# Performance work log

Measured on AMD Instinct MI355X. Metric: run time of the kernel, lower is better.

The kernel has to match this reference:

```python
import jax, jax.numpy as jnp
import numpy as np

INF = 1e+24
DK = 16


def setup_inputs() -> dict:
    key = jax.random.key(0)
    ks = jax.random.split(key, 9)
    B, T, D = 64, 512, 1024
    x = jax.random.normal(ks[0], (B, T, D), dtype=jnp.float32)
    padding_mask = jax.random.randint(ks[1], (B, T, 1), 0, 2) > 0
    s = 1.0 / np.sqrt(D)
    Wq = jax.random.normal(ks[2], (D, DK), dtype=jnp.float32) * s
    bq = jnp.zeros((DK,), dtype=jnp.float32)
    Wk = jax.random.normal(ks[3], (D, DK), dtype=jnp.float32) * s
    bk = jnp.zeros((DK,), dtype=jnp.float32)
    Wv = jax.random.normal(ks[4], (D, D), dtype=jnp.float32) * s
    bv = jnp.zeros((D,), dtype=jnp.float32)
    return {"x": x, "padding_mask": padding_mask, "Wq": Wq, "bq": bq,
            "Wk": Wk, "bk": bk, "Wv": Wv, "bv": bv}


def reference(x, padding_mask, Wq, bq, Wk, bk, Wv, bv):
    # x: [B,T,D]; padding_mask: [B,T,1] bool
    q = x @ Wq + bq                      # [B,T,dk]
    k = x @ Wk + bk                      # [B,T,dk]
    v = x @ Wv + bv                      # [B,T,D]
    # original writes -INF into k at padded positions (broadcast over dk)
    k = jnp.where(padding_mask, jnp.float32(-INF), k)
    # NOTE: original multiplies by sqrt(dk) (misnamed _inv_dk)
    att = jnp.einsum('btd,bsd->bts', q, k) * jnp.sqrt(jnp.float32(DK))
    T = x.shape[1]
    causal = jnp.triu(jnp.ones((T, T), dtype=bool), k=1)  # [T,T]
    att = jnp.where(causal[None, :, :], jnp.float32(-INF), att)
    return jnp.einsum('bts,bsd->btd', jax.nn.softmax(att, axis=2), v)
```

## Files before the change

kernel.cpp:

```cpp
#include <hip/hip_runtime.h>
#include <hip/hip_bf16.h>
#include <stdint.h>

#define NEG_BIG (-1e24f)

typedef __attribute__((ext_vector_type(8))) short bf16x8;
typedef __attribute__((ext_vector_type(4))) float f32x4;

#define AS1 __attribute__((address_space(1)))
#define AS3 __attribute__((address_space(3)))

__device__ __forceinline__ void gload_lds16(const void* g, void* l) {
    __builtin_amdgcn_global_load_lds((AS1 unsigned*)g, (AS3 unsigned*)l, 16, 0, 0);
}

__device__ __forceinline__ unsigned short f2bf(float f) {
    union { float f; unsigned u; } v; v.f = f;
    return (unsigned short)((v.u + 0x7FFFu + ((v.u >> 16) & 1u)) >> 16);
}

__global__ void detect_mask_kernel(const unsigned* pm, int* flag) {
    __shared__ int notI, notF;
    if (threadIdx.x == 0) { notI = 0; notF = 0; }
    __syncthreads();
    int li = 0, lf = 0;
    for (int i = threadIdx.x; i < 8192; i += 256) {
        unsigned v = pm[i];
        if (v > 1u) li = 1;
        if (v != 0u && v != 0x3F800000u) lf = 1;
    }
    if (li) atomicOr(&notI, 1);
    if (lf) atomicOr(&notF, 1);
    __syncthreads();
    if (threadIdx.x == 0) *flag = notI ? (notF ? 1 : 2) : 0;
}

__global__ __launch_bounds__(1024, 8)
void qk_conv_kernel(const float* __restrict__ x,
                    const float* __restrict__ Wq, const float* __restrict__ bq,
                    const float* __restrict__ Wk, const float* __restrict__ bk,
                    const void* __restrict__ pm, const int* __restrict__ pmflag,
                    unsigned short* __restrict__ xbf,
                    float* __restrict__ qo, float* __restrict__ ko) {
    __shared__ float smem[4 * 64 * 33];
    float* xs = smem;
    const int tid = threadIdx.x;
    const int r0 = blockIdx.x * 64;
    const int lane = tid & 63;
    const int wv = __builtin_amdgcn_readfirstlane(tid >> 6);
    const int g = wv & 3;
    const int sl = wv >> 2;
    const int jb = (g & 1) * 8;
    const int d0 = sl * 16;
    const float* __restrict__ W = (g < 2) ? Wq : Wk;

    const int sr = tid >> 4;
    const int sd = (tid & 15) * 4;
    const float* __restrict__ xp = x + (size_t)(r0 + sr) * 1024 + sd;
    unsigned short* __restrict__ xbp = xbf + (size_t)(r0 + sr) * 1024 + sd;

    float acc[8];
#pragma unroll
    for (int j = 0; j < 8; j++) acc[j] = 0.f;

    float4 xv = *(const float4*)xp;
    for (int c0 = 0; c0 < 1024; c0 += 64) {
        uint2 pk;
        pk.x = (unsigned)f2bf(xv.x) | ((unsigned)f2bf(xv.y) << 16);
        pk.y = (unsigned)f2bf(xv.z) | ((unsigned)f2bf(xv.w) << 16);
        *(uint2*)(xbp + c0) = pk;
        xs[sr * 65 + sd + 0] = xv.x;
        xs[sr * 65 + sd + 1] = xv.y;
        xs[sr * 65 + sd + 2] = xv.z;
        xs[sr * 65 + sd + 3] = xv.w;
        __syncthreads();
        if (c0 + 64 < 1024) xv = *(const float4*)(xp + c0 + 64);
        const float* __restrict__ wrow = W + (size_t)(c0 + d0) * 16 + jb;
        const float* __restrict__ xrow = xs + lane * 65 + d0;
#pragma unroll 4
        for (int dd = 0; dd < 16; dd++) {
            const float xvv = xrow[dd];
            const float* __restrict__ w = wrow + (size_t)dd * 16;
#pragma unroll
            for (int j = 0; j < 8; j++) acc[j] = fmaf(xvv, w[j], acc[j]);
        }
        __syncthreads();
    }

    float* red = smem;
    const int cb = jb + (g >> 1) * 16;
    {
        float* rr = red + ((size_t)(sl * 64 + lane)) * 33 + cb;
#pragma unroll
        for (int j = 0; j < 8; j++) rr[j] = acc[j];
    }
    __syncthreads();

    const int row = tid >> 4;
    const int c = tid & 15;
    const int grow = r0 + row;
    const float qv = red[(size_t)row * 33 + c]
                   + red[(size_t)(64 + row) * 33 + c]
                   + red[(size_t)(128 + row) * 33 + c]
                   + red[(size_t)(192 + row) * 33 + c] + bq[c];
    qo[(size_t)grow * 16 + c] = qv;
    const int flag = *pmflag;
    bool mk;
    if (flag == 1) mk = ((const unsigned char*)pm)[grow] != 0;
    else           mk = ((const unsigned*)pm)[grow] != 0;
    float kv;
    if (mk) {
        kv = NEG_BIG;
    } else {
        kv = red[(size_t)row * 33 + 16 + c]
           + red[(size_t)(64 + row) * 33 + 16 + c]
           + red[(size_t)(128 + row) * 33 + 16 + c]
           + red[(size_t)(192 + row) * 33 + 16 + c] + bk[c];
    }
    ko[(size_t)grow * 16 + c] = kv;
}

__global__ void wvt_kernel(const float* __restrict__ Wv, unsigned short* __restrict__ WvT) {
    __shared__ float tile[32][33];
    const int k0 = blockIdx.x * 32, n0 = blockIdx.y * 32;
    const int tid = threadIdx.x;
#pragma unroll
    for (int i = 0; i < 4; i++) {
        int idx = i * 256 + tid;
        int r = idx >> 5, c = idx & 31;
        tile[r][c] = Wv[(size_t)(k0 + r) * 1024 + n0 + c];
    }
    __syncthreads();
#pragma unroll
    for (int i = 0; i < 4; i++) {
        int idx = i * 256 + tid;
        int r = idx >> 5, c = idx & 31;
        WvT[(size_t)(n0 + r) * 1024 + k0 + c] = f2bf(tile[c][r]);
    }
}

__global__ __launch_bounds__(256, 2)
void vgemm_kernel(const unsigned short* __restrict__ A,
                  const unsigned short* __restrict__ Bt,
                  const float* __restrict__ bias,
                  unsigned short* __restrict__ vTg) {
    __shared__ __align__(16) unsigned short smem[17408];
    unsigned short* As = smem;
    unsigned short* Bs = smem + 4096;
    const int bid = blockIdx.x;
    const int c = bid & 7;
    const int g = bid >> 3;
    const int mt = c * 32 + (g >> 3);
    const int nt = g & 7;
    const int m0 = mt * 128;
    const int n0 = nt * 128;
    const int tid = threadIdx.x;
    const int lane = tid & 63;
    const int wave = tid >> 6;
    const int wm = (wave & 1) * 64;
    const int wn = (wave >> 1) * 64;
    const int l15 = lane & 15;
    const int quad = lane >> 4;
    const int arow = tid >> 2;
    const int acol = (tid & 3) * 8;
    f32x4 acc[4][4];
#pragma unroll
    for (int i = 0; i < 4; i++)
#pragma unroll
        for (int j = 0; j < 4; j++)
#pragma unroll
            for (int r = 0; r < 4; r++) acc[i][j][r] = 0.f;

    for (int k0 = 0; k0 < 1024; k0 += 32) {
        gload_lds16(A + (size_t)(m0 + arow) * 1024 + k0 + acol, As + tid * 8);
        gload_lds16(A + (size_t)(m0 + 64 + arow) * 1024 + k0 + acol, As + 2048 + tid * 8);
        gload_lds16(Bt + (size_t)(n0 + arow) * 1024 + k0 + acol, Bs + tid * 8);
        gload_lds16(Bt + (size_t)(n0 + 64 + arow) * 1024 + k0 + acol, Bs + 2048 + tid * 8);
        __syncthreads();
        bf16x8 af[4], bfr[4];
#pragma unroll
        for (int i = 0; i < 4; i++) {
            af[i]  = *(const bf16x8*)(As + (wm + i * 16 + l15) * 32 + quad * 8);
            bfr[i] = *(const bf16x8*)(Bs + (wn + i * 16 + l15) * 32 + quad * 8);
        }
#pragma unroll
        for (int i = 0; i < 4; i++)
#pragma unroll
            for (int j = 0; j < 4; j++)
                acc[i][j] = __builtin_amdgcn_mfma_f32_16x16x32_bf16(af[i], bfr[j], acc[i][j], 0, 0, 0);
        __syncthreads();
    }
    unsigned short* vt = smem;
#pragma unroll
    for (int j = 0; j < 4; j++) {
        const int e_local = wn + j * 16 + l15;
        const float bb = bias[n0 + e_local];
#pragma unroll
        for (int i = 0; i < 4; i++) {
            const int s_base = wm + i * 16 + quad * 4;
            unsigned short h0 = f2bf(acc[i][j][0] + bb);
            unsigned short h1 = f2bf(acc[i][j][1] + bb);
            unsigned short h2 = f2bf(acc[i][j][2] + bb);
            unsigned short h3 = f2bf(acc[i][j][3] + bb);
            uint2 u;
            u.x = (unsigned)h0 | ((unsigned)h1 << 16);
            u.y = (unsigned)h2 | ((unsigned)h3 << 16);
            *(uint2*)(vt + e_local * 136 + s_base) = u;
        }
    }
    __syncthreads();
    const int b = m0 >> 9;
    const int sbase = m0 & 511;
#pragma unroll
    for (int p = 0; p < 8; p++) {
        const int idx = p * 256 + tid;
        const int e = idx >> 4;
        const int s8 = (idx & 15) * 8;
        uint4 val = *(const uint4*)(vt + e * 136 + s8);
        *(uint4*)(vTg + ((size_t)b * 1024 + n0 + e) * 512 + sbase + s8) = val;
    }
}

__global__ __launch_bounds__(256, 2)
void score_kernel(const float* __restrict__ q, const float* __restrict__ k,
                  unsigned short* __restrict__ P, float* __restrict__ isum) {
    __shared__ float Kt[512 * 16];
    __shared__ float Qt[128 * 16];
    __shared__ float redm[2][128];
    __shared__ float reds[2][128];
    __shared__ unsigned short Pt[2][64][132];
    const int tid = threadIdx.x;
    const int b = blockIdx.y;
    const int t0 = blockIdx.x * 128;
    {
        const float4* ks = (const float4*)(k + (size_t)b * 512 * 16);
        float4* kd = (float4*)Kt;
#pragma unroll
        for (int i = 0; i < 8; i++) kd[i * 256 + tid] = ks[i * 256 + tid];
        const float4* qs = (const float4*)(q + ((size_t)b * 512 + t0) * 16);
        float4* qd = (float4*)Qt;
#pragma unroll
        for (int i = 0; i < 2; i++) qd[i * 256 + tid] = qs[i * 256 + tid];
    }
    __syncthreads();
    const int row = tid & 127;
    const int half = tid >> 7;
    const int sbeg = half * 256;
    const int tglob = t0 + row;
    float qr[16];
#pragma unroll
    for (int j = 0; j < 16; j++) qr[j] = Qt[row * 16 + j];

    float m = -INFINITY;
    for (int s = sbeg; s < sbeg + 256; s++) {
        const float* kk = Kt + s * 16;
        float dot = 0.f;
#pragma unroll
        for (int j = 0; j < 16; j++) dot = fmaf(qr[j], kk[j], dot);
        float sc = (s > tglob) ? NEG_BIG : dot * 4.0f;
        m = fmaxf(m, sc);
    }
    redm[half][row] = m;
    __syncthreads();
    const float M = fmaxf(redm[0][row], redm[1][row]);
    float sum = 0.f;
    for (int ph = 0; ph < 4; ph++) {
        const int c0 = sbeg + ph * 64;
        for (int s = c0; s < c0 + 64; s++) {
            const float* kk = Kt + s * 16;
            float dot = 0.f;
#pragma unroll
            for (int j = 0; j < 16; j++) dot = fmaf(qr[j], kk[j], dot);
            float sc = (s > tglob) ? NEG_BIG : dot * 4.0f;
            float p = __expf(sc - M);
            sum += p;
            Pt[half][s - c0][row] = f2bf(p);
        }
        __syncthreads();
#pragma unroll
        for (int i = 0; i < 8; i++) {
            int li = i * 256 + tid;
            int h = li >> 10;
            int r = (li >> 3) & 127;
            int cg = li & 7;
            union { unsigned short u[8]; uint4 v; } tmp;
#pragma unroll
            for (int j = 0; j < 8; j++) tmp.u[j] = Pt[h][cg * 8 + j][r];
            *(uint4*)(P + ((size_t)(b * 512 + t0 + r)) * 512 + h * 256 + ph * 64 + cg * 8) = tmp.v;
        }
        __syncthreads();
    }
    reds[half][row] = sum;
    __syncthreads();
    if (half == 0) {
        float tot = reds[0][row] + reds[1][row];
        isum[(size_t)b * 512 + tglob] = 1.0f / tot;
    }
}

__global__ __launch_bounds__(256, 2)
void pv_kernel(const unsigned short* __restrict__ P,
               const unsigned short* __restrict__ vT,
               const float* __restrict__ isum,
               float* __restrict__ out) {
    __shared__ unsigned short As[128 * 32];
    __shared__ unsigned short Bs[128 * 32];
    const int bid = blockIdx.x;
    const int c = bid & 7;
    const int g = bid >> 3;
    const int b = c * 8 + (g >> 5);
    const int rem = g & 31;
    const int m0 = (rem >> 3) * 128;
    const int n0 = (rem & 7) * 128;
    const int tid = threadIdx.x;
    const int lane = tid & 63;
    const int wave = tid >> 6;
    const int wm = (wave & 1) * 64;
    const int wn = (wave >> 1) * 64;
    const int l15 = lane & 15;
    const int quad = lane >> 4;
    const int arow = tid >> 2;
    const int acol = (tid & 3) * 8;
    const unsigned short* Ab = P + (size_t)b * 512 * 512;
    const unsigned short* Bb = vT + (size_t)b * 1024 * 512;
    f32x4 acc[4][4];
#pragma unroll
    for (int i = 0; i < 4; i++)
#pragma unroll
        for (int j = 0; j < 4; j++)
#pragma unroll
            for (int r = 0; r < 4; r++) acc[i][j][r] = 0.f;

    for (int k0 = 0; k0 < 512; k0 += 32) {
        gload_lds16(Ab + (size_t)(m0 + arow) * 512 + k0 + acol, As + tid * 8);
        gload_lds16(Ab + (size_t)(m0 + 64 + arow) * 512 + k0 + acol, As + 2048 + tid * 8);
        gload_lds16(Bb + (size_t)(n0 + arow) * 512 + k0 + acol, Bs + tid * 8);
        gload_lds16(Bb + (size_t)(n0 + 64 + arow) * 512 + k0 + acol, Bs + 2048 + tid * 8);
        __syncthreads();
        bf16x8 af[4], bfr[4];
#pragma unroll
        for (int i = 0; i < 4; i++) {
            af[i]  = *(const bf16x8*)(As + (wm + i * 16 + l15) * 32 + quad * 8);
            bfr[i] = *(const bf16x8*)(Bs + (wn + i * 16 + l15) * 32 + quad * 8);
        }
#pragma unroll
        for (int i = 0; i < 4; i++)
#pragma unroll
            for (int j = 0; j < 4; j++)
                acc[i][j] = __builtin_amdgcn_mfma_f32_16x16x32_bf16(af[i], bfr[j], acc[i][j], 0, 0, 0);
        __syncthreads();
    }
#pragma unroll
    for (int i = 0; i < 4; i++) {
#pragma unroll
        for (int r = 0; r < 4; r++) {
            const int trow = m0 + wm + i * 16 + quad * 4 + r;
            const float sc = isum[(size_t)b * 512 + trow];
#pragma unroll
            for (int j = 0; j < 4; j++) {
                const int ncol = n0 + wn + j * 16 + l15;
                out[((size_t)b * 512 + trow) * 1024 + ncol] = acc[i][j][r] * sc;
            }
        }
    }
}

extern "C" void kernel_launch(void* const* d_in, const int* in_sizes, int n_in,
                              void* d_out, int out_size, void* d_ws, size_t ws_size,
                              hipStream_t stream) {
    const float* x  = (const float*)d_in[0];
    const void*  pm = d_in[1];
    const float* Wq = (const float*)d_in[2];
    const float* bq = (const float*)d_in[3];
    const float* Wk = (const float*)d_in[4];
    const float* bk = (const float*)d_in[5];
    const float* Wv = (const float*)d_in[6];
    const float* bv = (const float*)d_in[7];
    float* out = (float*)d_out;

    char* ws = (char*)d_ws;
    const size_t MB = 1024 * 1024;
    unsigned short* xbf = (unsigned short*)ws;
    unsigned short* Pun = (unsigned short*)ws;
    unsigned short* vT  = (unsigned short*)(ws + 64 * MB);
    float* qbuf = (float*)(ws + 128 * MB);
    float* kbuf = (float*)(ws + 130 * MB);
    unsigned short* WvT = (unsigned short*)(ws + 132 * MB);
    float* isum = (float*)(ws + 134 * MB);
    int* flag   = (int*)(ws + 135 * MB);

    detect_mask_kernel<<<1, 256, 0, stream>>>((const unsigned*)pm, flag);
    qk_conv_kernel<<<512, 1024, 0, stream>>>(x, Wq, bq, Wk, bk, pm, flag, xbf, qbuf, kbuf);
    wvt_kernel<<<dim3(32, 32), 256, 0, stream>>>(Wv, WvT);
    vgemm_kernel<<<2048, 256, 0, stream>>>(xbf, WvT, bv, vT);
    score_kernel<<<dim3(4, 64), 256, 0, stream>>>(qbuf, kbuf, Pun, isum);
    pv_kernel<<<2048, 256, 0, stream>>>(Pun, vT, isum, out);
}
```

Before: 472.2 us.

## Double-buffer LDS tiles in V-GEMM and PV kernels, raise occupancy hint

Both GEMM kernels now use two LDS buffers, so the next K-tile's global-to-LDS load is issued before the MFMA work on the current tile. This lets memory latency hide behind compute instead of stalling at a barrier every iteration. Launch bounds go from 2 to 4 blocks per CU, which caps registers per thread. The per-iteration row pointers are also precomputed. The risks are register spills under the tighter launch bound and a larger LDS footprint, about 32KB per block.

Measured after the change: 467.5 us. Within noise of the previous version (-1.0%).

```diff
diff --git a/kernel.cpp b/kernel.cpp
--- a/kernel.cpp
+++ b/kernel.cpp
@@ -139,14 +139,12 @@
     }
 }
 
-__global__ __launch_bounds__(256, 2)
+__global__ __launch_bounds__(256, 4)
 void vgemm_kernel(const unsigned short* __restrict__ A,
                   const unsigned short* __restrict__ Bt,
                   const float* __restrict__ bias,
                   unsigned short* __restrict__ vTg) {
     __shared__ __align__(16) unsigned short smem[17408];
-    unsigned short* As = smem;
-    unsigned short* Bs = smem + 4096;
     const int bid = blockIdx.x;
     const int c = bid & 7;
     const int g = bid >> 3;
@@ -163,6 +161,10 @@
     const int quad = lane >> 4;
     const int arow = tid >> 2;
     const int acol = (tid & 3) * 8;
+    const unsigned short* __restrict__ Ar0 = A + (size_t)(m0 + arow) * 1024 + acol;
+    const unsigned short* __restrict__ Ar1 = A + (size_t)(m0 + 64 + arow) * 1024 + acol;
+    const unsigned short* __restrict__ Br0 = Bt + (size_t)(n0 + arow) * 1024 + acol;
+    const unsigned short* __restrict__ Br1 = Bt + (size_t)(n0 + 64 + arow) * 1024 + acol;
     f32x4 acc[4][4];
 #pragma unroll
     for (int i = 0; i < 4; i++)
@@ -171,12 +173,28 @@
 #pragma unroll
             for (int r = 0; r < 4; r++) acc[i][j][r] = 0.f;
 
-    for (int k0 = 0; k0 < 1024; k0 += 32) {
-        gload_lds16(A + (size_t)(m0 + arow) * 1024 + k0 + acol, As + tid * 8);
-        gload_lds16(A + (size_t)(m0 + 64 + arow) * 1024 + k0 + acol, As + 2048 + tid * 8);
-        gload_lds16(Bt + (size_t)(n0 + arow) * 1024 + k0 + acol, Bs + tid * 8);
-        gload_lds16(Bt + (size_t)(n0 + 64 + arow) * 1024 + k0 + acol, Bs + 2048 + tid * 8);
-        __syncthreads();
+    {
+        unsigned short* As = smem;
+        unsigned short* Bs = smem + 4096;
+        gload_lds16(Ar0, As + tid * 8);
+        gload_lds16(Ar1, As + 2048 + tid * 8);
+        gload_lds16(Br0, Bs + tid * 8);
+        gload_lds16(Br1, Bs + 2048 + tid * 8);
+    }
+    __syncthreads();
+    int cur = 0;
+    for (int t = 0; t < 32; t++) {
+        if (t + 1 < 32) {
+            const int kn = (t + 1) * 32;
+            unsigned short* As = smem + (cur ^ 1) * 8192;
+            unsigned short* Bs = As + 4096;
+            gload_lds16(Ar0 + kn, As + tid * 8);
+            gload_lds16(Ar1 + kn, As + 2048 + tid * 8);
+            gload_lds16(Br0 + kn, Bs + tid * 8);
+            gload_lds16(Br1 + kn, Bs + 2048 + tid * 8);
+        }
+        const unsigned short* As = smem + cur * 8192;
+        const unsigned short* Bs = As + 4096;
         bf16x8 af[4], bfr[4];
 #pragma unroll
         for (int i = 0; i < 4; i++) {
@@ -189,6 +207,7 @@
             for (int j = 0; j < 4; j++)
                 acc[i][j] = __builtin_amdgcn_mfma_f32_16x16x32_bf16(af[i], bfr[j], acc[i][j], 0, 0, 0);
         __syncthreads();
+        cur ^= 1;
     }
     unsigned short* vt = smem;
 #pragma unroll
@@ -298,13 +317,12 @@
     }
 }
 
-__global__ __launch_bounds__(256, 2)
+__global__ __launch_bounds__(256, 4)
 void pv_kernel(const unsigned short* __restrict__ P,
                const unsigned short* __restrict__ vT,
                const float* __restrict__ isum,
                float* __restrict__ out) {
-    __shared__ unsigned short As[128 * 32];
-    __shared__ unsigned short Bs[128 * 32];
+    __shared__ __align__(16) unsigned short smem[16384];
     const int bid = blockIdx.x;
     const int c = bid & 7;
     const int g = bid >> 3;
@@ -321,8 +339,10 @@
     const int quad = lane >> 4;
     const int arow = tid >> 2;
     const int acol = (tid & 3) * 8;
-    const unsigned short* Ab = P + (size_t)b * 512 * 512;
-    const unsigned short* Bb = vT + (size_t)b * 1024 * 512;
+    const unsigned short* __restrict__ Ar0 = P + (size_t)b * 512 * 512 + (size_t)(m0 + arow) * 512 + acol;
+    const unsigned short* __restrict__ Ar1 = Ar0 + (size_t)64 * 512;
+    const unsigned short* __restrict__ Br0 = vT + (size_t)b * 1024 * 512 + (size_t)(n0 + arow) * 512 + acol;
+    const unsigned short* __restrict__ Br1 = Br0 + (size_t)64 * 512;
     f32x4 acc[4][4];
 #pragma unroll
     for (int i = 0; i < 4; i++)
@@ -331,12 +351,28 @@
 #pragma unroll
             for (int r = 0; r < 4; r++) acc[i][j][r] = 0.f;
 
-    for (int k0 = 0; k0 < 512; k0 += 32) {
-        gload_lds16(Ab + (size_t)(m0 + arow) * 512 + k0 + acol, As + tid * 8);
-        gload_lds16(Ab + (size_t)(m0 + 64 + arow) * 512 + k0 + acol, As + 2048 + tid * 8);
-        gload_lds16(Bb + (size_t)(n0 + arow) * 512 + k0 + acol, Bs + tid * 8);
-        gload_lds16(Bb + (size_t)(n0 + 64 + arow) * 512 + k0 + acol, Bs + 2048 + tid * 8);
-        __syncthreads();
+    {
+        unsigned short* As = smem;
+        unsigned short* Bs = smem + 4096;
+        gload_lds16(Ar0, As + tid * 8);
+        gload_lds16(Ar1, As + 2048 + tid * 8);
+        gload_lds16(Br0, Bs + tid * 8);
+        gload_lds16(Br1, Bs + 2048 + tid * 8);
+    }
+    __syncthreads();
+    int cur = 0;
+    for (int t = 0; t < 16; t++) {
+        if (t + 1 < 16) {
+            const int kn = (t + 1) * 32;
+            unsigned short* As = smem + (cur ^ 1) * 8192;
+            unsigned short* Bs = As + 4096;
+            gload_lds16(Ar0 + kn, As + tid * 8);
+            gload_lds16(Ar1 + kn, As + 2048 + tid * 8);
+            gload_lds16(Br0 + kn, Bs + tid * 8);
+            gload_lds16(Br1 + kn, Bs + 2048 + tid * 8);
+        }
+        const unsigned short* As = smem + cur * 8192;
+        const unsigned short* Bs = As + 4096;
         bf16x8 af[4], bfr[4];
 #pragma unroll
         for (int i = 0; i < 4; i++) {
@@ -349,6 +385,7 @@
             for (int j = 0; j < 4; j++)
                 acc[i][j] = __builtin_amdgcn_mfma_f32_16x16x32_bf16(af[i], bfr[j], acc[i][j], 0, 0, 0);
         __syncthreads();
+        cur ^= 1;
     }
 #pragma unroll
     for (int i = 0; i < 4; i++) {
```
